# Performance work log

Measured on AMD Instinct MI355X. Metric: run time of the kernel, lower is better.

The kernel has to match this reference:

```python
import jax, jax.numpy as jnp
import numpy as np

D = 256  # subgraph_width
N_CLASSES = 10
EPS = 1e-5  # torch LayerNorm default


def _layernorm(x, g, b):
    mu = jnp.mean(x, axis=-1, keepdims=True)
    var = jnp.var(x, axis=-1, keepdims=True)
    return (x - mu) * jax.lax.rsqrt(var + EPS) * g + b


def setup_inputs() -> dict:
    key = jax.random.key(0)
    ks = jax.random.split(key, 16)
    B, T, N = 64, 512, 512
    traj = jax.random.normal(ks[0], (B, T, 2), dtype=jnp.float32)
    labels = jax.random.randint(ks[1], (B,), 0, N_CLASSES)
    h = jax.random.normal(ks[2], (B, N, D), dtype=jnp.float32)
    valid_len = jnp.maximum(jax.random.randint(ks[3], (B,), 0, N), 1)
    s = 0.02
    params = dict(
        emb=jax.random.normal(ks[4], (N_CLASSES, D), dtype=jnp.float32) * s,
        w_mlp=jax.random.normal(ks[5], (2, D), dtype=jnp.float32) * s,
        b_mlp=jnp.zeros((D,), jnp.float32),
        ln_g=jnp.ones((D,), jnp.float32),
        ln_b=jnp.zeros((D,), jnp.float32),
        wq=jax.random.normal(ks[6], (D, D), dtype=jnp.float32) * s,
        bq=jnp.zeros((D,), jnp.float32),
        wk=jax.random.normal(ks[7], (D, D), dtype=jnp.float32) * s,
        bk=jnp.zeros((D,), jnp.float32),
        wv=jax.random.normal(ks[8], (D, D), dtype=jnp.float32) * s,
        bv=jnp.zeros((D,), jnp.float32),
        w_out=jax.random.normal(ks[9], (D, 1), dtype=jnp.float32) * s,
        b_out=jnp.zeros((1,), jnp.float32),
    )
    return dict(traj=traj, labels=labels, h=h, valid_len=valid_len, **params)


def reference(traj, labels, h, valid_len, emb, w_mlp, b_mlp, ln_g, ln_b,
              wq, bq, wk, bk, wv, bv, w_out, b_out):
    # MLP(in=2, out=D, activation='leaky'): Linear -> LayerNorm -> LeakyReLU
    x = jax.nn.leaky_relu(_layernorm(traj @ w_mlp + b_mlp, ln_g, ln_b))  # [B,T,D]
    le = emb[labels]                          # [B,D]
    x = x + le[:, None, :]                    # embed-add
    # SelfAttentionWithKeyFCLayer: Q from x, K/V from h, scaled, key-masked by valid_len
    q = x @ wq + bq                            # [B,T,D]
    k = h @ wk + bk                            # [B,N,D]
    v = h @ wv + bv                            # [B,N,D]
    scores = jnp.einsum('btd,bnd->btn', q, k) / jnp.sqrt(jnp.float32(D))
    N = h.shape[1]
    key_mask = jnp.arange(N)[None, :] < valid_len[:, None]          # [B,N]
    scores = jnp.where(key_mask[:, None, :], scores, jnp.float32(-1e9))
    attn = jax.nn.softmax(scores, axis=-1)
    enc = jnp.einsum('btn,bnd->btd', attn, v)  # [B,T,D]
    pooled = jnp.max(enc, axis=1) + le          # [B,D]
    return jax.nn.sigmoid(pooled @ w_out + b_out)  # [B,1]
```

## Files before the change

kernel.cpp:

```cpp
#include <hip/hip_runtime.h>
#include <math.h>

typedef float f32x4 __attribute__((ext_vector_type(4)));
typedef __bf16 bf16x8 __attribute__((ext_vector_type(8)));
typedef unsigned short u16x8 __attribute__((ext_vector_type(8)));
typedef unsigned short u16x4 __attribute__((ext_vector_type(4)));
typedef unsigned int u32x4 __attribute__((ext_vector_type(4)));

#define MFMA(a, b, c) __builtin_amdgcn_mfma_f32_16x16x32_bf16((a), (b), (c), 0, 0, 0)

static __device__ __forceinline__ unsigned short f2bf(float f) {
  unsigned u = __float_as_uint(f);
  u += 0x7FFFu + ((u >> 16) & 1u);
  return (unsigned short)(u >> 16);
}
static __device__ __forceinline__ float bf2f(unsigned short s) {
  return __uint_as_float(((unsigned)s) << 16);
}
static __device__ __forceinline__ unsigned cvt_pk(float lo, float hi) {
  unsigned r;
  asm("v_cvt_pk_bf16_f32 %0, %1, %2" : "=v"(r) : "v"(lo), "v"(hi));
  return r;
}

static __device__ __forceinline__ int swz512(int row, int col) {
  return row * 512 + (col ^ ((((row & 7) ^ (col >> 6)) & 7) << 4));
}
static __device__ __forceinline__ int swzV(int d, int col) {
  return d * 64 + (col ^ (((d >> 1) & 3) << 4));
}
static __device__ __forceinline__ int swzO64(int d, int col) {
  return d * 128 + (col ^ ((d & 7) << 4));
}

__global__ __launch_bounds__(256) void setup(
    const float* __restrict__ w0m, const float* __restrict__ w1m, const float* __restrict__ w2m,
    unsigned short* __restrict__ t0m, unsigned short* __restrict__ t1m, unsigned short* __restrict__ t2m,
    const float* __restrict__ w_mlp, const float* __restrict__ b_mlp, float* __restrict__ lnsc,
    const int* __restrict__ vlen, int* __restrict__ tasktab) {
  int bid = blockIdx.x;
  int t = threadIdx.x;
  if (bid == 48) {
    float w0 = w_mlp[t], w1 = w_mlp[256 + t], bb = b_mlp[t];
    float v[9] = {w0, w1, bb, w0 * w0, w1 * w1, w0 * w1, w0 * bb, w1 * bb, bb * bb};
    __shared__ float red[4][9];
#pragma unroll
    for (int j = 0; j < 9; ++j) {
      float s = v[j];
#pragma unroll
      for (int off = 32; off >= 1; off >>= 1) s += __shfl_xor(s, off, 64);
      v[j] = s;
    }
    if ((t & 63) == 0)
      for (int j = 0; j < 9; ++j) red[t >> 6][j] = v[j];
    __syncthreads();
    if (t < 9) lnsc[t] = red[0][t] + red[1][t] + red[2][t] + red[3][t];
    return;
  }
  if (bid == 49) {
    __shared__ int srank[64];
    if (t < 64) {
      int vb = vlen[t], r = 0;
      for (int j = 0; j < 64; ++j) {
        int vj = vlen[j];
        r += (vj > vb) || (vj == vb && j < t);
      }
      srank[r] = t;
    }
    __syncthreads();
    if (t < 64) {
      int r = t;
      int b1 = srank[r];
      int b2 = srank[63 - r];
      int xcd = r & 7, a = r >> 3;
      for (int tt = 0; tt < 4; ++tt) {
        tasktab[(a * 4 + tt) * 8 + xcd] = (b1 << 3) | tt;
        tasktab[256 + (a * 4 + tt) * 8 + xcd] = (b2 << 3) | (tt + 4);
      }
    }
    return;
  }
  int m = bid >> 4, t16 = bid & 15;
  const float* w = (m == 0) ? w0m : (m == 1) ? w1m : w2m;
  unsigned short* o = (m == 0) ? t0m : (m == 1) ? t1m : t2m;
  __shared__ float sm[64][65];
  int bi = t16 >> 2, bj = t16 & 3;
  for (int kb = 0; kb < 16; ++kb) {
    int idx = kb * 256 + t;
    int r = idx >> 6, c = idx & 63;
    sm[r][c] = w[(bi * 64 + r) * 256 + bj * 64 + c];
  }
  __syncthreads();
  for (int kb = 0; kb < 16; ++kb) {
    int idx = kb * 256 + t;
    int r = idx >> 6, c = idx & 63;
    int d = bj * 64 + r, e = bi * 64 + c;
    o[(e >> 5) * 8192 + d * 32 + (e & 31)] = f2bf(sm[c][r]);
  }
}

static __device__ __forceinline__ void gemm_direct(
    const unsigned short* __restrict__ Bpk, const unsigned short* Alds,
    int w, int g, int c15, f32x4 (&acc)[4][4]) {
  const unsigned short* bp = Bpk + (w * 64 + c15) * 32 + 8 * g;
#pragma unroll
  for (int c = 0; c < 8; ++c) {
    bf16x8 bfv[4];
#pragma unroll
    for (int nt = 0; nt < 4; ++nt)
      bfv[nt] = *(const bf16x8*)(bp + c * 8192 + nt * 512);
    bf16x8 af[4];
#pragma unroll
    for (int at = 0; at < 4; ++at)
      af[at] = *(const bf16x8*)((char*)Alds + swz512(at * 16 + c15, c * 64 + 16 * g));
    __builtin_amdgcn_s_setprio(1);
#pragma unroll
    for (int at = 0; at < 4; ++at)
#pragma unroll
      for (int nt = 0; nt < 4; ++nt) acc[at][nt] = MFMA(af[at], bfv[nt], acc[at][nt]);
    __builtin_amdgcn_s_setprio(0);
  }
}

__global__ __launch_bounds__(512, 4) void gemms(
    const float* __restrict__ h, const int* __restrict__ vlen,
    const unsigned short* __restrict__ wkPk, const float* __restrict__ bk,
    const unsigned short* __restrict__ wvPk, const float* __restrict__ bv,
    unsigned short* __restrict__ kout, unsigned short* __restrict__ vT) {
  __shared__ unsigned short Alds[64 * 256];
  __shared__ unsigned short Klds[64 * 256];
  int tid = threadIdx.x, w = tid >> 6, lane = tid & 63, g = lane >> 4, c15 = lane & 15;
  int tile = blockIdx.x;
  int b = tile >> 3;
  int nbase = (tile & 7) * 64;
  if (nbase >= vlen[b]) return;
  f32x4 acc[4][4];
  {
    const float* hb = h + (size_t)tile * 16384;
    f32x4 ha[4], hc[4];
#pragma unroll
    for (int i = 0; i < 4; ++i) {
      ha[i] = *(const f32x4*)(hb + i * 4096 + tid * 8);
      hc[i] = *(const f32x4*)(hb + i * 4096 + tid * 8 + 4);
    }
#pragma unroll
    for (int i = 0; i < 4; ++i) {
      u16x8 pk;
#pragma unroll
      for (int j = 0; j < 4; ++j) { pk[j] = f2bf(ha[i][j]); pk[j + 4] = f2bf(hc[i][j]); }
      *(u16x8*)((char*)Alds + swz512(i * 16 + (tid >> 5), (tid & 31) * 16)) = pk;
    }
  }
#pragma unroll
  for (int a = 0; a < 4; ++a)
#pragma unroll
    for (int n = 0; n < 4; ++n) acc[a][n] = (f32x4){0.f, 0.f, 0.f, 0.f};
  __syncthreads();

  int w4 = w & 3;
  if (w < 4) {
    gemm_direct(wvPk, Alds, w4, g, c15, acc);
#pragma unroll
    for (int at = 0; at < 4; ++at)
#pragma unroll
      for (int nt = 0; nt < 4; ++nt) {
        int col = w4 * 64 + nt * 16 + c15;
        float bb = bv[col];
        u16x4 o;
#pragma unroll
        for (int r = 0; r < 4; ++r) o[r] = f2bf(acc[at][nt][r] + bb);
        *(u16x4*)(vT + (size_t)b * 131072 + (size_t)col * 512 + nbase + at * 16 + 4 * g) = o;
      }
  } else {
    gemm_direct(wkPk, Alds, w4, g, c15, acc);
#pragma unroll
    for (int at = 0; at < 4; ++at)
#pragma unroll
      for (int nt = 0; nt < 4; ++nt) {
        int col = w4 * 64 + nt * 16 + c15;
        float bb = bk[col];
#pragma unroll
        for (int r = 0; r < 4; ++r)
          *(unsigned short*)((char*)Klds + swz512(at * 16 + 4 * g + r, col * 2)) =
              f2bf(acc[at][nt][r] + bb);
      }
  }
  __syncthreads();
  if (tid < 256) {
    int row = tid >> 2;
    for (int i = 0; i < 8; ++i) {
      int colb = (tid & 3) * 128 + i * 16;
      u16x8 vv = *(const u16x8*)((char*)Klds + swz512(row, colb));
      *(u16x8*)(kout + (size_t)(tile * 64 + row) * 256 + colb / 2) = vv;
    }
  }
}

__global__ __launch_bounds__(256, 2) void attn(
    const float* __restrict__ traj, const int* __restrict__ labels,
    const float* __restrict__ emb, const float* __restrict__ w_mlp,
    const float* __restrict__ b_mlp, const float* __restrict__ ln_g,
    const float* __restrict__ ln_b, const float* __restrict__ lnsc,
    const unsigned short* __restrict__ wqPk, const float* __restrict__ bq,
    const unsigned short* __restrict__ k, const unsigned short* __restrict__ vT,
    const int* __restrict__ valid_len, const int* __restrict__ tasktab,
    float* __restrict__ partial) {
  __shared__ unsigned short buf[2][16384];

  int task = tasktab[blockIdx.x];
  int b = task >> 3, tt = task & 7;
  int tid = threadIdx.x, w = tid >> 6, lane = tid & 63, g = lane >> 4, c15 = lane & 15;
  int vl = valid_len[b];
  int nit = (vl + 31) >> 5;

  {
    int rrow = tid >> 5, cb = (tid & 31) * 8;
    int lab = labels[b];
    f32x4 wa0 = *(const f32x4*)(w_mlp + cb), wa1 = *(const f32x4*)(w_mlp + cb + 4);
    f32x4 wb0 = *(const f32x4*)(w_mlp + 256 + cb), wb1 = *(const f32x4*)(w_mlp + 256 + cb + 4);
    f32x4 bm0 = *(const f32x4*)(b_mlp + cb), bm1 = *(const f32x4*)(b_mlp + cb + 4);
    f32x4 g0 = *(const f32x4*)(ln_g + cb), g1 = *(const f32x4*)(ln_g + cb + 4);
    f32x4 lb0 = *(const f32x4*)(ln_b + cb), lb1 = *(const f32x4*)(ln_b + cb + 4);
    f32x4 le0 = *(const f32x4*)(emb + lab * 256 + cb), le1 = *(const f32x4*)(emb + lab * 256 + cb + 4);
    float s0 = lnsc[0], s1 = lnsc[1], s2 = lnsc[2], s3 = lnsc[3], s4_ = lnsc[4],
          s5 = lnsc[5], s6 = lnsc[6], s7 = lnsc[7], s8 = lnsc[8];
#pragma unroll
    for (int i = 0; i < 8; ++i) {
      int row = i * 8 + rrow, grow = b * 512 + tt * 64 + row;
      float t0 = traj[grow * 2], t1 = traj[grow * 2 + 1];
      float mu = (t0 * s0 + t1 * s1 + s2) * (1.f / 256.f);
      float ea2 = (t0 * t0 * s3 + t1 * t1 * s4_ + s8 +
                   2.f * (t0 * t1 * s5 + t0 * s6 + t1 * s7)) * (1.f / 256.f);
      float rstd = rsqrtf(ea2 - mu * mu + 1e-5f);
      u16x8 pk;
#pragma unroll
      for (int j = 0; j < 4; ++j) {
        float a0 = t0 * wa0[j] + t1 * wb0[j] + bm0[j];
        float y0 = (a0 - mu) * rstd * g0[j] + lb0[j];
        pk[j] = f2bf((y0 > 0.f ? y0 : 0.01f * y0) + le0[j]);
        float a1 = t0 * wa1[j] + t1 * wb1[j] + bm1[j];
        float y1 = (a1 - mu) * rstd * g1[j] + lb1[j];
        pk[j + 4] = f2bf((y1 > 0.f ? y1 : 0.01f * y1) + le1[j]);
      }
      *(u16x8*)((char*)buf + swz512(row, cb * 2)) = pk;
    }
  }
  __syncthreads();

  {
    f32x4 qacc[4][4];
#pragma unroll
    for (int a = 0; a < 4; ++a)
#pragma unroll
      for (int n = 0; n < 4; ++n) qacc[a][n] = (f32x4){0.f, 0.f, 0.f, 0.f};
    gemm_direct(wqPk, (const unsigned short*)buf, w, g, c15, qacc);
    __syncthreads();
#pragma unroll
    for (int nt = 0; nt < 4; ++nt) {
      int col = w * 64 + nt * 16 + c15;
      float bb = bq[col];
#pragma unroll
      for (int at = 0; at < 4; ++at)
#pragma unroll
        for (int r = 0; r < 4; ++r)
          *(unsigned short*)((char*)buf + 32768 + swz512(at * 16 + 4 * g + r, col * 2)) =
              f2bf(qacc[at][nt][r] + bb);
    }
  }
  __syncthreads();
  bf16x8 qf[8];
#pragma unroll
  for (int kk = 0; kk < 8; ++kk)
    qf[kk] = *(const bf16x8*)((char*)buf + 32768 + swz512(w * 16 + c15, kk * 64 + 16 * g));
  __syncthreads();

  f32x4 acco[16];
#pragma unroll
  for (int i = 0; i < 16; ++i) acco[i] = (f32x4){0.f, 0.f, 0.f, 0.f};
  float rs = 0.f;

  const unsigned short* kbase = k + (size_t)b * 512 * 256;
  const unsigned short* vbase = vT + (size_t)b * 131072;
  u16x8 kpre[4], vpre[4];

#pragma unroll
  for (int i = 0; i < 4; ++i) {
    int idx = tid + 256 * i, key = idx >> 5, s = idx & 31;
    kpre[i] = *(const u16x8*)(kbase + (size_t)key * 256 + s * 8);
  }
#pragma unroll
  for (int i = 0; i < 4; ++i) {
    int idx = tid + 256 * i, d = idx >> 2, s = idx & 3;
    vpre[i] = *(const u16x8*)(vbase + (size_t)d * 512 + s * 8);
  }
#pragma unroll
  for (int i = 0; i < 4; ++i) {
    int idx = tid + 256 * i, key = idx >> 5, s = idx & 31;
    *(u16x8*)((char*)buf[0] + swz512(key, s * 16)) = kpre[i];
  }
#pragma unroll
  for (int i = 0; i < 4; ++i) {
    int idx = tid + 256 * i, d = idx >> 2, s = idx & 3;
    *(u16x8*)((char*)(buf[0] + 8192) + swzV(d, s * 16)) = vpre[i];
  }

  for (int it = 0; it < nit; ++it) {
    int cur = it & 1;
    __syncthreads();
    bool pf = (it + 1 < nit);
    if (pf) {
      int n1 = (it + 1) * 32;
#pragma unroll
      for (int i = 0; i < 4; ++i) {
        int idx = tid + 256 * i, key = idx >> 5, s = idx & 31;
        kpre[i] = *(const u16x8*)(kbase + (size_t)(n1 + key) * 256 + s * 8);
      }
#pragma unroll
      for (int i = 0; i < 4; ++i) {
        int idx = tid + 256 * i, d = idx >> 2, s = idx & 3;
        vpre[i] = *(const u16x8*)(vbase + (size_t)d * 512 + n1 + s * 8);
      }
    }
    unsigned short* Klds = buf[cur];
    unsigned short* Vlds = buf[cur] + 8192;
    int n0 = it * 32;

    float p[2][4];
    unsigned u01[2], u23[2];
#pragma unroll
    for (int c = 0; c < 2; ++c) {
      f32x4 s4 = (f32x4){0.f, 0.f, 0.f, 0.f};
      __builtin_amdgcn_s_setprio(1);
#pragma unroll
      for (int kk = 0; kk < 8; ++kk) {
        bf16x8 kf = *(const bf16x8*)((char*)Klds + swz512(c * 16 + c15, kk * 64 + 16 * g));
        s4 = MFMA(kf, qf[kk], s4);
      }
      __builtin_amdgcn_s_setprio(0);
#pragma unroll
      for (int r = 0; r < 4; ++r) {
        int key = n0 + c * 16 + 4 * g + r;
        float pv = (key < vl) ? __expf(s4[r] * 0.0625f) : 0.f;
        p[c][r] = pv;
        rs += pv;
      }
      u01[c] = cvt_pk(p[c][0], p[c][1]);
      u23[c] = cvt_pk(p[c][2], p[c][3]);
    }
    int srcA = c15 | ((lane & 16) << 1);
    int srcB = srcA + 16;
    unsigned x0a = (unsigned)__shfl((int)u01[0], srcA, 64);
    unsigned x1a = (unsigned)__shfl((int)u01[1], srcA, 64);
    unsigned x0b = (unsigned)__shfl((int)u23[0], srcA, 64);
    unsigned x1b = (unsigned)__shfl((int)u23[1], srcA, 64);
    unsigned x0c = (unsigned)__shfl((int)u01[0], srcB, 64);
    unsigned x1c = (unsigned)__shfl((int)u01[1], srcB, 64);
    unsigned x0d = (unsigned)__shfl((int)u23[0], srcB, 64);
    unsigned x1d = (unsigned)__shfl((int)u23[1], srcB, 64);
    bool hi = g >= 2;
    union { u32x4 u; bf16x8 v; } pa;
    pa.u[0] = hi ? x1a : x0a;
    pa.u[1] = hi ? x1b : x0b;
    pa.u[2] = hi ? x1c : x0c;
    pa.u[3] = hi ? x1d : x0d;
    __builtin_amdgcn_s_setprio(1);
#pragma unroll
    for (int dt = 0; dt < 16; ++dt) {
      bf16x8 vf = *(const bf16x8*)((char*)Vlds + swzV(dt * 16 + c15, 16 * g));
      acco[dt] = MFMA(vf, pa.v, acco[dt]);
    }
    __builtin_amdgcn_s_setprio(0);
    if (pf) {
      unsigned short* Kn = buf[cur ^ 1];
      unsigned short* Vn = buf[cur ^ 1] + 8192;
#pragma unroll
      for (int i = 0; i < 4; ++i) {
        int idx = tid + 256 * i, key = idx >> 5, s = idx & 31;
        *(u16x8*)((char*)Kn + swz512(key, s * 16)) = kpre[i];
      }
#pragma unroll
      for (int i = 0; i < 4; ++i) {
        int idx = tid + 256 * i, d = idx >> 2, s = idx & 3;
        *(u16x8*)((char*)Vn + swzV(d, s * 16)) = vpre[i];
      }
    }
  }
  rs += __shfl_xor(rs, 16, 64);
  rs += __shfl_xor(rs, 32, 64);
  float inv = 1.f / rs;
  __syncthreads();
  int qcol = w * 16 + c15;
#pragma unroll
  for (int dt = 0; dt < 16; ++dt)
#pragma unroll
    for (int r = 0; r < 4; ++r) {
      int d = dt * 16 + 4 * g + r;
      *(unsigned short*)((char*)buf + swzO64(d, qcol * 2)) = f2bf(acco[dt][r] * inv);
    }
  __syncthreads();
  {
    int d = tid;
    float m = -1e30f;
    for (int i = 0; i < 8; ++i) {
      u16x8 vv = *(const u16x8*)((char*)buf + swzO64(d, i * 16));
#pragma unroll
      for (int j = 0; j < 8; ++j) m = fmaxf(m, bf2f(vv[j]));
    }
    partial[((size_t)b * 8 + tt) * 256 + d] = m;
  }
}

__global__ __launch_bounds__(256) void finalize(
    const float* __restrict__ partial, const float* __restrict__ emb,
    const int* __restrict__ labels, const float* __restrict__ w_out,
    const float* __restrict__ b_out, float* __restrict__ out) {
  int b = blockIdx.x, t = threadIdx.x;
  float m = -1e30f;
#pragma unroll
  for (int s8 = 0; s8 < 8; ++s8)
    m = fmaxf(m, partial[((size_t)b * 8 + s8) * 256 + t]);
  m += emb[labels[b] * 256 + t];
  __shared__ float red[256];
  red[t] = m * w_out[t];
  __syncthreads();
  for (int s = 128; s > 0; s >>= 1) {
    if (t < s) red[t] += red[t + s];
    __syncthreads();
  }
  if (t == 0) out[b] = 1.f / (1.f + __expf(-(red[0] + b_out[0])));
}

extern "C" void kernel_launch(void* const* d_in, const int* in_sizes, int n_in,
                              void* d_out, int out_size, void* d_ws, size_t ws_size,
                              hipStream_t stream) {
  const float* traj   = (const float*)d_in[0];
  const int*   labels = (const int*)d_in[1];
  const float* h      = (const float*)d_in[2];
  const int*   vlen   = (const int*)d_in[3];
  const float* emb    = (const float*)d_in[4];
  const float* w_mlp  = (const float*)d_in[5];
  const float* b_mlp  = (const float*)d_in[6];
  const float* ln_g   = (const float*)d_in[7];
  const float* ln_b   = (const float*)d_in[8];
  const float* wq     = (const float*)d_in[9];
  const float* bq     = (const float*)d_in[10];
  const float* wk     = (const float*)d_in[11];
  const float* bk     = (const float*)d_in[12];
  const float* wv     = (const float*)d_in[13];
  const float* bv     = (const float*)d_in[14];
  const float* w_out  = (const float*)d_in[15];
  const float* b_out  = (const float*)d_in[16];
  float* out = (float*)d_out;

  unsigned short* kb   = (unsigned short*)d_ws;
  unsigned short* vT   = kb + (size_t)32768 * 256;
  unsigned short* wqPk = vT + (size_t)32768 * 256;
  unsigned short* wkPk = wqPk + 65536;
  unsigned short* wvPk = wkPk + 65536;
  float* lnsc    = (float*)(wvPk + 65536);
  float* partial = lnsc + 16;
  int*   tasktab = (int*)(partial + 64 * 8 * 256);

  setup<<<50, 256, 0, stream>>>(wq, wk, wv, wqPk, wkPk, wvPk, w_mlp, b_mlp, lnsc,
                                vlen, tasktab);
  gemms<<<512, 512, 0, stream>>>(h, vlen, wkPk, bk, wvPk, bv, kb, vT);
  attn<<<512, 256, 0, stream>>>(traj, labels, emb, w_mlp, b_mlp, ln_g, ln_b, lnsc,
                                wqPk, bq, kb, vT, vlen, tasktab, partial);
  finalize<<<64, 256, 0, stream>>>(partial, emb, labels, w_out, b_out, out);
}
```

Measured before the change: 68.81 us.

## Split long-key attention tiles across two blocks and merge with combine kernel

Batches with valid_len above 256 now have each query tile's key range split into two halves processed by separate blocks, which write unnormalized fp32 accumulators and row sums to workspace. A new combine kernel sums the halves, normalizes, and takes the max over queries. The task table is rebuilt per XCD with sentinel entries for padding. This aims to balance work across CUs, at the cost of extra global traffic for partial accumulators and an extra kernel launch.

Measured after the change: 113.5 us. 64.9% more time.

```diff
diff --git a/kernel.cpp b/kernel.cpp
--- a/kernel.cpp
+++ b/kernel.cpp
@@ -68,15 +68,17 @@
       srank[r] = t;
     }
     __syncthreads();
-    if (t < 64) {
-      int r = t;
-      int b1 = srank[r];
-      int b2 = srank[63 - r];
-      int xcd = r & 7, a = r >> 3;
-      for (int tt = 0; tt < 4; ++tt) {
-        tasktab[(a * 4 + tt) * 8 + xcd] = (b1 << 3) | tt;
-        tasktab[256 + (a * 4 + tt) * 8 + xcd] = (b2 << 3) | (tt + 4);
-      }
+    if (t < 8) {
+      int xcd = t, pos = 0;
+      for (int a = 0; a < 8; ++a) {
+        int r = a * 8 + xcd;
+        int b = srank[r];
+        int split = (vlen[b] > 256) ? 1 : 0;
+        for (int tt = 0; tt < 8; ++tt)
+          for (int hf = 0; hf <= split; ++hf)
+            tasktab[(pos++) * 8 + xcd] = (b << 5) | (tt << 2) | (hf << 1) | split;
+      }
+      for (; pos < 128; ++pos) tasktab[pos * 8 + xcd] = -1;
     }
     return;
   }
@@ -204,14 +206,17 @@
     const unsigned short* __restrict__ wqPk, const float* __restrict__ bq,
     const unsigned short* __restrict__ k, const unsigned short* __restrict__ vT,
     const int* __restrict__ valid_len, const int* __restrict__ tasktab,
-    float* __restrict__ partial) {
+    float* __restrict__ partial, float* __restrict__ pacc, float* __restrict__ prs) {
   __shared__ unsigned short buf[2][16384];
 
   int task = tasktab[blockIdx.x];
-  int b = task >> 3, tt = task & 7;
+  if (task < 0) return;
+  int b = task >> 5, tt = (task >> 2) & 7, half = (task >> 1) & 1, split = task & 1;
   int tid = threadIdx.x, w = tid >> 6, lane = tid & 63, g = lane >> 4, c15 = lane & 15;
   int vl = valid_len[b];
   int nit = (vl + 31) >> 5;
+  int c0 = (split && half) ? 8 : 0;
+  int c1 = (split && !half) ? 8 : nit;
 
   {
     int rrow = tid >> 5, cb = (tid & 31) * 8;
@@ -286,12 +291,12 @@
 #pragma unroll
   for (int i = 0; i < 4; ++i) {
     int idx = tid + 256 * i, key = idx >> 5, s = idx & 31;
-    kpre[i] = *(const u16x8*)(kbase + (size_t)key * 256 + s * 8);
+    kpre[i] = *(const u16x8*)(kbase + (size_t)(c0 * 32 + key) * 256 + s * 8);
   }
 #pragma unroll
   for (int i = 0; i < 4; ++i) {
     int idx = tid + 256 * i, d = idx >> 2, s = idx & 3;
-    vpre[i] = *(const u16x8*)(vbase + (size_t)d * 512 + s * 8);
+    vpre[i] = *(const u16x8*)(vbase + (size_t)d * 512 + c0 * 32 + s * 8);
   }
 #pragma unroll
   for (int i = 0; i < 4; ++i) {
@@ -304,10 +309,10 @@
     *(u16x8*)((char*)(buf[0] + 8192) + swzV(d, s * 16)) = vpre[i];
   }
 
-  for (int it = 0; it < nit; ++it) {
+  for (int it = c0; it < c1; ++it) {
     int cur = it & 1;
     __syncthreads();
-    bool pf = (it + 1 < nit);
+    bool pf = (it + 1 < c1);
     if (pf) {
       int n1 = (it + 1) * 32;
 #pragma unroll
@@ -387,6 +392,21 @@
   }
   rs += __shfl_xor(rs, 16, 64);
   rs += __shfl_xor(rs, 32, 64);
+
+  if (split) {
+    float* pa = pacc + (((size_t)b * 8 + tt) * 2 + half) * 16384;
+    int q = w * 16 + c15;
+#pragma unroll
+    for (int dt = 0; dt < 16; ++dt)
+#pragma unroll
+      for (int r = 0; r < 4; ++r) {
+        int d = dt * 16 + 4 * g + r;
+        pa[d * 64 + q] = acco[dt][r];
+      }
+    if (lane < 16) prs[(((size_t)b * 8 + tt) * 2 + half) * 64 + w * 16 + lane] = rs;
+    return;
+  }
+
   float inv = 1.f / rs;
   __syncthreads();
   int qcol = w * 16 + c15;
@@ -407,6 +427,25 @@
       for (int j = 0; j < 8; ++j) m = fmaxf(m, bf2f(vv[j]));
     }
     partial[((size_t)b * 8 + tt) * 256 + d] = m;
+  }
+}
+
+__global__ __launch_bounds__(256) void combine(
+    const float* __restrict__ pacc, const float* __restrict__ prs,
+    const int* __restrict__ vlen, float* __restrict__ partial) {
+  int bt = blockIdx.x;
+  int b = bt >> 3;
+  if (vlen[b] <= 256) return;
+  int tid = threadIdx.x, w = tid >> 6, lane = tid & 63;
+  const float* pa0 = pacc + (size_t)bt * 2 * 16384;
+  const float* pa1 = pa0 + 16384;
+  float invq = 1.f / (prs[(size_t)bt * 128 + lane] + prs[(size_t)bt * 128 + 64 + lane]);
+  for (int dd = 0; dd < 64; ++dd) {
+    int d = dd * 4 + w;
+    float o = (pa0[d * 64 + lane] + pa1[d * 64 + lane]) * invq;
+#pragma unroll
+    for (int off = 32; off >= 1; off >>= 1) o = fmaxf(o, __shfl_xor(o, off, 64));
+    if (lane == 0) partial[(size_t)bt * 256 + d] = o;
   }
 }
 
@@ -460,11 +499,14 @@
   float* lnsc    = (float*)(wvPk + 65536);
   float* partial = lnsc + 16;
   int*   tasktab = (int*)(partial + 64 * 8 * 256);
+  float* pacc    = (float*)(tasktab + 1024);
+  float* prs     = pacc + (size_t)64 * 8 * 2 * 16384;
 
   setup<<<50, 256, 0, stream>>>(wq, wk, wv, wqPk, wkPk, wvPk, w_mlp, b_mlp, lnsc,
                                 vlen, tasktab);
   gemms<<<512, 512, 0, stream>>>(h, vlen, wkPk, bk, wvPk, bv, kb, vT);
-  attn<<<512, 256, 0, stream>>>(traj, labels, emb, w_mlp, b_mlp, ln_g, ln_b, lnsc,
-                                wqPk, bq, kb, vT, vlen, tasktab, partial);
+  attn<<<1024, 256, 0, stream>>>(traj, labels, emb, w_mlp, b_mlp, ln_g, ln_b, lnsc,
+                                 wqPk, bq, kb, vT, vlen, tasktab, partial, pacc, prs);
+  combine<<<512, 256, 0, stream>>>(pacc, prs, vlen, partial);
   finalize<<<64, 256, 0, stream>>>(partial, emb, labels, w_out, b_out, out);
 }
```
